# Kernel tuning notes

Measured on AMD Instinct MI355X. Metric: run time of the kernel, lower is better.

The kernel has to match this reference:

```python
import jax, jax.numpy as jnp
import numpy as np

K = 4          # neighbor_num
BN_EPS = 1e-5


def setup_inputs() -> dict:
    key = jax.random.key(0)
    ks = jax.random.split(key, 5)
    b, n, c = 16384, 12, 512
    x = jax.random.normal(ks[0], (b, n, c), dtype=jnp.float32)
    std = np.sqrt(2.0 / c).astype(np.float32)
    Uw = jax.random.normal(ks[1], (c, c), dtype=jnp.float32) * std
    Vw = jax.random.normal(ks[2], (c, c), dtype=jnp.float32) * std
    bound = 1.0 / np.sqrt(c)
    Ub = jax.random.uniform(ks[3], (c,), minval=-bound, maxval=bound, dtype=jnp.float32)
    Vb = jax.random.uniform(ks[4], (c,), minval=-bound, maxval=bound, dtype=jnp.float32)
    gamma = jnp.ones((n,), dtype=jnp.float32)
    beta = jnp.zeros((n,), dtype=jnp.float32)
    return {"x": x, "Uw": Uw, "Ub": Ub, "Vw": Vw, "Vb": Vb, "gamma": gamma, "beta": beta}


def reference(x, Uw, Ub, Vw, Vb, gamma, beta):
    # x: [b, n, c] with n = num_classes nodes
    # ---- dynamic top-k adjacency ('dots' metric), built on detached x ----
    si = jax.lax.stop_gradient(x)
    sim = jnp.einsum('bic,bjc->bij', si, si)                 # [b, n, n]
    thr = jax.lax.top_k(sim, K)[0][..., -1:]                 # k-th largest per row
    adj = (sim >= thr).astype(x.dtype)                       # [b, n, n]
    # ---- normalize_digraph: D^{-1/2} A D^{-1/2} (row degrees) ----
    deg_inv_sqrt = adj.sum(axis=-1) ** -0.5                  # [b, n]
    A = deg_inv_sqrt[:, :, None] * adj * deg_inv_sqrt[:, None, :]
    # ---- aggregate + projections ----
    Vx = jnp.einsum('bnc,dc->bnd', x, Vw) + Vb               # V(x)
    agg = jnp.einsum('bij,bjc->bic', A, Vx)
    h = agg + jnp.einsum('bnc,dc->bnd', x, Uw) + Ub          # aggregate + U(x)
    # ---- BatchNorm1d over node channel n (stats over batch and feature dims) ----
    mean = h.mean(axis=(0, 2))                               # [n]
    var = ((h - mean[None, :, None]) ** 2).mean(axis=(0, 2)) # biased var, [n]
    hn = (h - mean[None, :, None]) * jax.lax.rsqrt(var + BN_EPS)[None, :, None]
    hn = hn * gamma[None, :, None] + beta[None, :, None]
    return jax.nn.relu(x + hn)
```

## Files before the change

### kernel.cpp

```cpp
#include <hip/hip_runtime.h>
#include <hip/hip_fp16.h>


typedef _Float16 half8 __attribute__((ext_vector_type(8)));
typedef float floatx4 __attribute__((ext_vector_type(4)));

#define NN 12
#define CH 512
#define NB 16384
#define M_ROWS (NB * NN)

__device__ __forceinline__ float relu_f(float v) { return v > 0.f ? v : 0.f; }

__global__ __launch_bounds__(256) void kw_build(const float* __restrict__ Uw,
                                                const float* __restrict__ Vw,
                                                _Float16* __restrict__ Wcat,
                                                double* __restrict__ gAcc) {
    int e = blockIdx.x * 256 + threadIdx.x;
    int d = e >> 10, k = e & 1023;
    float v = (k < 512) ? Uw[d * 512 + k] : Vw[d * 512 + (k - 512)];
    Wcat[e] = (_Float16)v;
    if (blockIdx.x == 0 && threadIdx.x < 24) gAcc[threadIdx.x] = 0.0;
}

__global__ __launch_bounds__(256) void k1_adj(const float* __restrict__ x,
                                              _Float16* __restrict__ Abuf,
                                              float* __restrict__ rs,
                                              int pathA) {
    __shared__ float xs[NN][CH + 1];
    __shared__ double sim[NN][NN];
    __shared__ double thr[NN];
    __shared__ float Amat[NN][NN];
    __shared__ float dinv[NN];

    const int b = blockIdx.x, t = threadIdx.x;
    const float* xb = x + (size_t)b * NN * CH;

    for (int e = t; e < NN * CH / 4; e += 256) {
        int r = e >> 7, c4 = (e & 127) << 2;
        float4 v = ((const float4*)xb)[e];
        xs[r][c4 + 0] = v.x; xs[r][c4 + 1] = v.y;
        xs[r][c4 + 2] = v.z; xs[r][c4 + 3] = v.w;
    }
    __syncthreads();

    if (t < 144) {
        int i = t / 12, j = t % 12;
        double acc = 0.0;
        for (int c = 0; c < CH; c++) acc += (double)xs[i][c] * (double)xs[j][c];
        sim[i][j] = acc;
    }
    __syncthreads();

    if (t < 12) {
        double a = -1e300, b2 = -1e300, c2 = -1e300, d2 = -1e300;
        for (int j = 0; j < 12; j++) {
            double v = sim[t][j];
            if (v > a)       { d2 = c2; c2 = b2; b2 = a; a = v; }
            else if (v > b2) { d2 = c2; c2 = b2; b2 = v; }
            else if (v > c2) { d2 = c2; c2 = v; }
            else if (v > d2) { d2 = v; }
        }
        thr[t] = d2;
        int deg = 0;
        for (int j = 0; j < 12; j++) deg += (sim[t][j] >= d2);
        dinv[t] = 1.0f / sqrtf((float)deg);
    }
    __syncthreads();

    if (t < 144) {
        int i = t / 12, j = t % 12;
        Amat[i][j] = (sim[i][j] >= thr[i]) ? dinv[i] * dinv[j] : 0.0f;
    }
    __syncthreads();

    if (t < 12) {
        float s = 0.f;
        for (int j = 0; j < 12; j++) s += Amat[t][j];
        rs[b * NN + t] = s;
    }

    const size_t strideK = pathA ? 1024 : 512;
    const size_t yoff = pathA ? 512 : 0;
    for (int e = t; e < NN * CH; e += 256) {
        int i = e >> 9, c = e & 511;
        float acc = 0.f;
#pragma unroll
        for (int j = 0; j < 12; j++) acc += Amat[i][j] * xs[j][c];
        size_t row = (size_t)b * NN + i;
        Abuf[row * strideK + yoff + c] = (_Float16)acc;
        if (pathA) Abuf[row * strideK + c] = (_Float16)xs[i][c];
    }
}

__global__ __launch_bounds__(256) void k2_gemm(
    const _Float16* __restrict__ Abuf, const float* __restrict__ xf,
    const _Float16* __restrict__ Wcat, const float* __restrict__ rs,
    const float* __restrict__ Ub, const float* __restrict__ Vb,
    float* __restrict__ hout, double* __restrict__ gS1,
    double* __restrict__ gS2, int pathA) {
    __shared__ __align__(16) _Float16 As[128 * 32];
    __shared__ __align__(16) _Float16 Bs[128 * 32];
    __shared__ float bs1[12], bs2[12];

    const int t = threadIdx.x;
    const int mt = blockIdx.x >> 2, nt = blockIdx.x & 3;
    const int m0 = mt * 128, n0 = nt * 128;
    const int lane = t & 63, wv = t >> 6;
    const int l15 = lane & 15, quad = lane >> 4;
    const int mwb = (wv & 1) * 64, nwb = (wv >> 1) * 64;
    const int srow = t >> 2, scol = (t & 3) * 8;

    floatx4 acc[4][4];
#pragma unroll
    for (int mi = 0; mi < 4; mi++)
#pragma unroll
        for (int ni = 0; ni < 4; ni++)
#pragma unroll
            for (int e = 0; e < 4; e++) acc[mi][ni][e] = 0.f;

    for (int kt = 0; kt < 32; kt++) {
        const int k0 = kt * 32;
        __syncthreads();
#pragma unroll
        for (int pass = 0; pass < 2; pass++) {
            const int row = srow + pass * 64;
            const size_t grow = (size_t)(m0 + row);
            half8 va;
            if (pathA) {
                va = *(const half8*)(Abuf + grow * 1024 + k0 + scol);
            } else if (k0 < 512) {
                const float* p = xf + grow * 512 + k0 + scol;
                float4 f0 = *(const float4*)p;
                float4 f1 = *(const float4*)(p + 4);
                va[0] = (_Float16)f0.x; va[1] = (_Float16)f0.y;
                va[2] = (_Float16)f0.z; va[3] = (_Float16)f0.w;
                va[4] = (_Float16)f1.x; va[5] = (_Float16)f1.y;
                va[6] = (_Float16)f1.z; va[7] = (_Float16)f1.w;
            } else {
                va = *(const half8*)(Abuf + grow * 512 + (k0 - 512) + scol);
            }
            *(half8*)&As[row * 32 + scol] = va;
            half8 vb = *(const half8*)(Wcat + (size_t)(n0 + row) * 1024 + k0 + scol);
            *(half8*)&Bs[row * 32 + scol] = vb;
        }
        __syncthreads();

        half8 af[4], bfr[4];
#pragma unroll
        for (int mi = 0; mi < 4; mi++)
            af[mi] = *(half8*)&As[(mwb + mi * 16 + l15) * 32 + quad * 8];
#pragma unroll
        for (int ni = 0; ni < 4; ni++)
            bfr[ni] = *(half8*)&Bs[(nwb + ni * 16 + l15) * 32 + quad * 8];
#pragma unroll
        for (int mi = 0; mi < 4; mi++)
#pragma unroll
            for (int ni = 0; ni < 4; ni++)
                acc[mi][ni] = __builtin_amdgcn_mfma_f32_16x16x32_f16(
                    af[mi], bfr[ni], acc[mi][ni], 0, 0, 0);
    }

    if (t < 12) { bs1[t] = 0.f; bs2[t] = 0.f; }
    __syncthreads();
#pragma unroll
    for (int mi = 0; mi < 4; mi++) {
#pragma unroll
        for (int r = 0; r < 4; r++) {
            const int m = m0 + mwb + mi * 16 + quad * 4 + r;
            const float rsm = rs[m];
            float p1 = 0.f, p2 = 0.f;
#pragma unroll
            for (int ni = 0; ni < 4; ni++) {
                const int d = n0 + nwb + ni * 16 + l15;
                float h = acc[mi][ni][r] + rsm * Vb[d] + Ub[d];
                hout[(size_t)m * 512 + d] = h;
                p1 += h; p2 += h * h;
            }
            for (int off = 1; off < 16; off <<= 1) {
                p1 += __shfl_xor(p1, off, 16);
                p2 += __shfl_xor(p2, off, 16);
            }
            if (l15 == 0) {
                atomicAdd(&bs1[m % 12], p1);
                atomicAdd(&bs2[m % 12], p2);
            }
        }
    }
    __syncthreads();
    if (t < 12) {
        atomicAdd(&gS1[t], (double)bs1[t]);
        atomicAdd(&gS2[t], (double)bs2[t]);
    }
}

__global__ void k3_stats(const double* __restrict__ gS1,
                         const double* __restrict__ gS2,
                         const float* __restrict__ gamma,
                         const float* __restrict__ beta,
                         float* __restrict__ bnp) {
    int t = threadIdx.x;
    if (t < 12) {
        const double cnt = (double)NB * 512.0;
        double mean = gS1[t] / cnt;
        double var = gS2[t] / cnt - mean * mean;
        float inv = rsqrtf((float)var + 1e-5f);
        float scale = gamma[t] * inv;
        bnp[t] = scale;
        bnp[12 + t] = beta[t] - (float)mean * scale;
    }
}

__global__ __launch_bounds__(256) void k4_final(const float* __restrict__ x,
                                                float* __restrict__ out,
                                                const float* __restrict__ bnp) {
    __shared__ float sc[12], sh[12];
    if (threadIdx.x < 12) {
        sc[threadIdx.x] = bnp[threadIdx.x];
        sh[threadIdx.x] = bnp[12 + threadIdx.x];
    }
    __syncthreads();
    const size_t n4 = (size_t)M_ROWS * 128;
    for (size_t i = (size_t)blockIdx.x * 256 + threadIdx.x; i < n4;
         i += (size_t)gridDim.x * 256) {
        int m = (int)(i >> 7);
        int n = m % 12;
        float4 h = ((const float4*)out)[i];
        float4 xv = ((const float4*)x)[i];
        float s = sc[n], b = sh[n];
        float4 r;
        r.x = relu_f(xv.x + h.x * s + b);
        r.y = relu_f(xv.y + h.y * s + b);
        r.z = relu_f(xv.z + h.z * s + b);
        r.w = relu_f(xv.w + h.w * s + b);
        ((float4*)out)[i] = r;
    }
}

extern "C" void kernel_launch(void* const* d_in, const int* in_sizes, int n_in,
                              void* d_out, int out_size, void* d_ws,
                              size_t ws_size, hipStream_t stream) {
    const float* x     = (const float*)d_in[0];
    const float* Uw    = (const float*)d_in[1];
    const float* Ub    = (const float*)d_in[2];
    const float* Vw    = (const float*)d_in[3];
    const float* Vb    = (const float*)d_in[4];
    const float* gamma = (const float*)d_in[5];
    const float* beta  = (const float*)d_in[6];
    float* out = (float*)d_out;

    const size_t szA  = (size_t)M_ROWS * 1024 * 2;
    const size_t szB  = (size_t)M_ROWS * 512 * 2;
    const size_t szW  = (size_t)512 * 1024 * 2;
    const size_t szrs = (size_t)M_ROWS * 4;
    const size_t needA = szA + szW + szrs + 24 * 8 + 24 * 4;
    const int pathA = (ws_size >= needA) ? 1 : 0;

    char* w = (char*)d_ws;
    _Float16* Abuf = (_Float16*)w;
    const size_t big = pathA ? szA : szB;
    _Float16* Wcat = (_Float16*)(w + big);
    float* rs      = (float*)(w + big + szW);
    double* gS1    = (double*)(w + big + szW + szrs);
    double* gS2    = gS1 + 12;
    float* bnp     = (float*)(gS2 + 12);

    kw_build<<<2048, 256, 0, stream>>>(Uw, Vw, Wcat, gS1);
    k1_adj<<<NB, 256, 0, stream>>>(x, Abuf, rs, pathA);
    k2_gemm<<<(M_ROWS / 128) * 4, 256, 0, stream>>>(Abuf, x, Wcat, rs, Ub, Vb,
                                                    out, gS1, gS2, pathA);
    k3_stats<<<1, 64, 0, stream>>>(gS1, gS2, gamma, beta, bnp);
    k4_final<<<4096, 256, 0, stream>>>(x, out, bnp);
}
```

Measured before the change: 1.532 ms.

## Use direct global-to-LDS loads in GEMM, XCD-aware tile mapping, vectorize adjacency kernel

The GEMM staging loads are replaced with global_load_lds builtins that write straight into LDS, so the data no longer passes through registers. Block IDs are remapped so M tiles are spread across XCDs, which is meant to improve L2 locality for shared weight and activation tiles. The adjacency kernel now computes only the upper triangle of the similarity matrix and vectorizes its LDS reads and fp16 stores with float4/half4. The per-wave LDS offset layout for global_load_lds depends on lane-contiguous writes, so a wrong mapping could corrupt the staged tiles.

```diff
diff --git a/kernel.cpp b/kernel.cpp
--- a/kernel.cpp
+++ b/kernel.cpp
@@ -3,6 +3,7 @@
 
 
 typedef _Float16 half8 __attribute__((ext_vector_type(8)));
+typedef _Float16 half4 __attribute__((ext_vector_type(4)));
 typedef float floatx4 __attribute__((ext_vector_type(4)));
 
 #define NN 12
@@ -11,6 +12,12 @@
 #define M_ROWS (NB * NN)
 
 __device__ __forceinline__ float relu_f(float v) { return v > 0.f ? v : 0.f; }
+
+__device__ __forceinline__ void gload16(const void* g, void* l) {
+    __builtin_amdgcn_global_load_lds(
+        (__attribute__((address_space(1))) const unsigned int*)g,
+        (__attribute__((address_space(3))) unsigned int*)l, 16, 0, 0);
+}
 
 __global__ __launch_bounds__(256) void kw_build(const float* __restrict__ Uw,
                                                 const float* __restrict__ Vw,
@@ -27,7 +34,7 @@
                                               _Float16* __restrict__ Abuf,
                                               float* __restrict__ rs,
                                               int pathA) {
-    __shared__ float xs[NN][CH + 1];
+    __shared__ float xs[NN][CH + 4];
     __shared__ double sim[NN][NN];
     __shared__ double thr[NN];
     __shared__ float Amat[NN][NN];
@@ -39,16 +46,26 @@
     for (int e = t; e < NN * CH / 4; e += 256) {
         int r = e >> 7, c4 = (e & 127) << 2;
         float4 v = ((const float4*)xb)[e];
-        xs[r][c4 + 0] = v.x; xs[r][c4 + 1] = v.y;
-        xs[r][c4 + 2] = v.z; xs[r][c4 + 3] = v.w;
-    }
-    __syncthreads();
-
-    if (t < 144) {
-        int i = t / 12, j = t % 12;
-        double acc = 0.0;
-        for (int c = 0; c < CH; c++) acc += (double)xs[i][c] * (double)xs[j][c];
+        *(float4*)&xs[r][c4] = v;
+    }
+    __syncthreads();
+
+    if (t < 78) {
+        int i = 0, rem = t;
+        while (rem >= NN - i) { rem -= NN - i; i++; }
+        const int j = i + rem;
+        double a0 = 0.0, a1 = 0.0, a2 = 0.0, a3 = 0.0;
+        for (int c = 0; c < CH; c += 4) {
+            float4 va = *(const float4*)&xs[i][c];
+            float4 vb = *(const float4*)&xs[j][c];
+            a0 += (double)va.x * (double)vb.x;
+            a1 += (double)va.y * (double)vb.y;
+            a2 += (double)va.z * (double)vb.z;
+            a3 += (double)va.w * (double)vb.w;
+        }
+        double acc = (a0 + a1) + (a2 + a3);
         sim[i][j] = acc;
+        sim[j][i] = acc;
     }
     __syncthreads();
 
@@ -82,14 +99,27 @@
 
     const size_t strideK = pathA ? 1024 : 512;
     const size_t yoff = pathA ? 512 : 0;
-    for (int e = t; e < NN * CH; e += 256) {
-        int i = e >> 9, c = e & 511;
-        float acc = 0.f;
-#pragma unroll
-        for (int j = 0; j < 12; j++) acc += Amat[i][j] * xs[j][c];
-        size_t row = (size_t)b * NN + i;
-        Abuf[row * strideK + yoff + c] = (_Float16)acc;
-        if (pathA) Abuf[row * strideK + c] = (_Float16)xs[i][c];
+    for (int e = t; e < NN * CH / 4; e += 256) {
+        int i = e >> 7, c4 = (e & 127) << 2;
+        float ax = 0.f, ay = 0.f, az = 0.f, aw = 0.f;
+#pragma unroll
+        for (int j = 0; j < 12; j++) {
+            const float a = Amat[i][j];
+            float4 v = *(const float4*)&xs[j][c4];
+            ax += a * v.x; ay += a * v.y; az += a * v.z; aw += a * v.w;
+        }
+        const size_t row = (size_t)b * NN + i;
+        half4 hy;
+        hy[0] = (_Float16)ax; hy[1] = (_Float16)ay;
+        hy[2] = (_Float16)az; hy[3] = (_Float16)aw;
+        *(half4*)(Abuf + row * strideK + yoff + c4) = hy;
+        if (pathA) {
+            float4 xv = *(const float4*)&xs[i][c4];
+            half4 hx;
+            hx[0] = (_Float16)xv.x; hx[1] = (_Float16)xv.y;
+            hx[2] = (_Float16)xv.z; hx[3] = (_Float16)xv.w;
+            *(half4*)(Abuf + row * 1024 + c4) = hx;
+        }
     }
 }
 
@@ -104,13 +134,18 @@
     __shared__ float bs1[12], bs2[12];
 
     const int t = threadIdx.x;
-    const int mt = blockIdx.x >> 2, nt = blockIdx.x & 3;
+    const int bid = blockIdx.x;
+    const int xcd = bid & 7, jj = bid >> 3;
+    const int nt = jj & 3, mt = (jj >> 2) * 8 + xcd;
     const int m0 = mt * 128, n0 = nt * 128;
     const int lane = t & 63, wv = t >> 6;
     const int l15 = lane & 15, quad = lane >> 4;
     const int mwb = (wv & 1) * 64, nwb = (wv >> 1) * 64;
     const int srow = t >> 2, scol = (t & 3) * 8;
 
+    _Float16* ldsA = As + wv * 512;
+    _Float16* ldsB = Bs + wv * 512;
+
     floatx4 acc[4][4];
 #pragma unroll
     for (int mi = 0; mi < 4; mi++)
@@ -122,27 +157,37 @@
     for (int kt = 0; kt < 32; kt++) {
         const int k0 = kt * 32;
         __syncthreads();
-#pragma unroll
-        for (int pass = 0; pass < 2; pass++) {
-            const int row = srow + pass * 64;
-            const size_t grow = (size_t)(m0 + row);
-            half8 va;
-            if (pathA) {
-                va = *(const half8*)(Abuf + grow * 1024 + k0 + scol);
-            } else if (k0 < 512) {
-                const float* p = xf + grow * 512 + k0 + scol;
-                float4 f0 = *(const float4*)p;
-                float4 f1 = *(const float4*)(p + 4);
-                va[0] = (_Float16)f0.x; va[1] = (_Float16)f0.y;
-                va[2] = (_Float16)f0.z; va[3] = (_Float16)f0.w;
-                va[4] = (_Float16)f1.x; va[5] = (_Float16)f1.y;
-                va[6] = (_Float16)f1.z; va[7] = (_Float16)f1.w;
-            } else {
-                va = *(const half8*)(Abuf + grow * 512 + (k0 - 512) + scol);
-            }
-            *(half8*)&As[row * 32 + scol] = va;
-            half8 vb = *(const half8*)(Wcat + (size_t)(n0 + row) * 1024 + k0 + scol);
-            *(half8*)&Bs[row * 32 + scol] = vb;
+        if (pathA) {
+#pragma unroll
+            for (int pass = 0; pass < 2; pass++) {
+                const int row = srow + pass * 64;
+                const size_t grow = (size_t)(m0 + row);
+                gload16(Abuf + grow * 1024 + k0 + scol, ldsA + pass * 2048);
+                gload16(Wcat + (size_t)(n0 + row) * 1024 + k0 + scol,
+                        ldsB + pass * 2048);
+            }
+        } else {
+#pragma unroll
+            for (int pass = 0; pass < 2; pass++) {
+                const int row = srow + pass * 64;
+                const size_t grow = (size_t)(m0 + row);
+                if (k0 < 512) {
+                    const float* p = xf + grow * 512 + k0 + scol;
+                    float4 f0 = *(const float4*)p;
+                    float4 f1 = *(const float4*)(p + 4);
+                    half8 va;
+                    va[0] = (_Float16)f0.x; va[1] = (_Float16)f0.y;
+                    va[2] = (_Float16)f0.z; va[3] = (_Float16)f0.w;
+                    va[4] = (_Float16)f1.x; va[5] = (_Float16)f1.y;
+                    va[6] = (_Float16)f1.z; va[7] = (_Float16)f1.w;
+                    *(half8*)&As[row * 32 + scol] = va;
+                } else {
+                    gload16(Abuf + grow * 512 + (k0 - 512) + scol,
+                            ldsA + pass * 2048);
+                }
+                gload16(Wcat + (size_t)(n0 + row) * 1024 + k0 + scol,
+                        ldsB + pass * 2048);
+            }
         }
         __syncthreads();
 
```

Result: faster. 1.413 ms (-7.8%).
